# Kernel optimization log

Measured on AMD Instinct MI355X. Metric: run time of the kernel, lower is better.

Reference implementation:

```python
import jax, jax.numpy as jnp
import numpy as np

B, N, F, H, L = 8, 512, 32, 64, 2

def setup_inputs() -> dict:
    key = jax.random.key(0)
    ks = jax.random.split(key, 16)
    s = lambda fan_in: 1.0 / np.sqrt(fan_in)
    return {
        "x": jax.random.normal(ks[0], (B, N, F), dtype=jnp.float32),
        # node encoder: Linear(F, H), stored as [in, out]
        "W_enc": jax.random.uniform(ks[1], (F, H), minval=-s(F), maxval=s(F)),
        "b_enc": jax.random.uniform(ks[2], (H,), minval=-s(F), maxval=s(F)),
        # edge MLP: Linear(2H, H) then Linear(H, 1)
        "W_e1": jax.random.uniform(ks[3], (2 * H, H), minval=-s(2 * H), maxval=s(2 * H)),
        "b_e1": jax.random.uniform(ks[4], (H,), minval=-s(2 * H), maxval=s(2 * H)),
        "W_e2": jax.random.uniform(ks[5], (H,), minval=-s(H), maxval=s(H)),
        "b_e2": jax.random.uniform(ks[6], (), minval=-s(H), maxval=s(H)),
        # per-layer message Linear(H, H)
        "W_msg": jax.random.uniform(ks[7], (L, H, H), minval=-s(H), maxval=s(H)),
        "b_msg": jax.random.uniform(ks[8], (L, H), minval=-s(H), maxval=s(H)),
        # per-layer GRUCell(H, H): gates ordered [r, z, n], stored as [in, 3H]
        "W_ih": jax.random.uniform(ks[9], (L, H, 3 * H), minval=-s(H), maxval=s(H)),
        "b_ih": jax.random.uniform(ks[10], (L, 3 * H), minval=-s(H), maxval=s(H)),
        "W_hh": jax.random.uniform(ks[11], (L, H, 3 * H), minval=-s(H), maxval=s(H)),
        "b_hh": jax.random.uniform(ks[12], (L, 3 * H), minval=-s(H), maxval=s(H)),
        # output Linear(H, 1)
        "W_out": jax.random.uniform(ks[13], (H, 1), minval=-s(H), maxval=s(H)),
        "b_out": jax.random.uniform(ks[14], (1,), minval=-s(H), maxval=s(H)),
    }

def reference(x, W_enc, b_enc, W_e1, b_e1, W_e2, b_e2, W_msg, b_msg,
              W_ih, b_ih, W_hh, b_hh, W_out, b_out):
    # Node encoding (dropout is eval-mode identity)
    h = jax.nn.relu(x @ W_enc + b_enc)  # [B, N, H]

    # Edge MLP on pairwise concat [h_i, h_j]: split W_e1 so we never build the 2H concat
    Wa, Wb = W_e1[:H], W_e1[H:]
    zi = h @ Wa                           # contribution of h_i, [B, N, H]
    zj = h @ Wb                           # contribution of h_j, [B, N, H]
    e = jax.nn.relu(zi[:, :, None, :] + zj[:, None, :, :] + b_e1)  # [B, N, N, H]
    logits = jnp.einsum('bijh,h->bij', e, W_e2) + b_e2             # [B, N, N]

    eye = jnp.eye(logits.shape[-1], dtype=bool)
    logits = jnp.where(eye[None], -jnp.inf, logits)
    adj = jax.nn.softmax(logits, axis=-1)
    adj = jnp.nan_to_num(adj, nan=0.0, posinf=0.0, neginf=0.0)

    for l in range(L):
        m = jnp.einsum('bij,bjh->bih', adj, h)             # message aggregation
        m = jax.nn.relu(m @ W_msg[l] + b_msg[l])
        # GRUCell update (gates [r, z, n])
        gi = m @ W_ih[l] + b_ih[l]
        gh = h @ W_hh[l] + b_hh[l]
        ir, iz, inn = jnp.split(gi, 3, axis=-1)
        hr, hz, hn = jnp.split(gh, 3, axis=-1)
        r = jax.nn.sigmoid(ir + hr)
        z = jax.nn.sigmoid(iz + hz)
        n = jnp.tanh(inn + r * hn)
        h = (1.0 - z) * n + z * h

    graph_emb = jnp.mean(h, axis=1)       # [B, H]
    return graph_emb @ W_out + b_out      # [B, 1]
```

## Files before the change

kernel.cpp:

```cpp
#include <hip/hip_runtime.h>
#include <math.h>

#define BB 8
#define NN 512
#define FF 32
#define HH 64
#define NEG_BIG (-1.0e30f)

__device__ __forceinline__ float lane_bcast(float v, int l) {
    return __int_as_float(__builtin_amdgcn_readlane(__float_as_int(v), l));
}

__global__ __launch_bounds__(256) void encode_kernel(
    const float* __restrict__ x, const float* __restrict__ W_enc,
    const float* __restrict__ b_enc, const float* __restrict__ W_e1,
    const float* __restrict__ b_e1,
    float* __restrict__ h, float* __restrict__ zi, float* __restrict__ zj)
{
    const int t = threadIdx.x;
    const int hh = t & 63;
    const int qu = __builtin_amdgcn_readfirstlane(t >> 6);
    const int gR = blockIdx.x * 4 + qu;

    const float xv = x[gR * FF + (hh & 31)];
    float acc = b_enc[hh];
#pragma unroll 8
    for (int k = 0; k < FF; ++k)
        acc = fmaf(lane_bcast(xv, k), W_enc[k * HH + hh], acc);
    const float hval = fmaxf(acc, 0.f);
    h[gR * HH + hh] = hval;

    float z1 = b_e1[hh], z2 = 0.f;
#pragma unroll 8
    for (int k = 0; k < HH; ++k) {
        const float hk = lane_bcast(hval, k);
        z1 = fmaf(hk, W_e1[k * HH + hh], z1);
        z2 = fmaf(hk, W_e1[(HH + k) * HH + hh], z2);
    }
    zi[gR * HH + hh] = z1;
    zj[gR * HH + hh] = z2;
}

__global__ __launch_bounds__(256) void adj_kernel(
    const float* __restrict__ zi, const float* __restrict__ zj,
    const float* __restrict__ W_e2, const float* __restrict__ b_e2,
    float* __restrict__ adj)
{
    const int b = blockIdx.x >> 7;
    const int i0 = (blockIdx.x & 127) << 2;
    const int t = threadIdx.x;
    const int qu = __builtin_amdgcn_readfirstlane(t >> 6);
    const int tj = t & 63;
    const int j0 = (qu << 7) + tj;
    const int j1 = j0 + 64;

    __shared__ float zjs[NN][17];
    __shared__ float red[4][8];

    float zr[4];
#pragma unroll
    for (int r = 0; r < 4; ++r) zr[r] = zi[(b * NN + i0 + r) * HH + tj];
    const float wv = W_e2[tj];

    const float be2 = b_e2[0];
    float acc0[4], acc1[4];
#pragma unroll
    for (int r = 0; r < 4; ++r) { acc0[r] = be2; acc1[r] = be2; }

    for (int kp = 0; kp < 4; ++kp) {
        __syncthreads();
        {
            const int idx4 = t;
#pragma unroll
            for (int u = 0; u < 8; ++u) {
                const int i4 = idx4 + u * 256;
                const int row = i4 >> 2, c4 = i4 & 3;
                *(float4*)&zjs[row][c4 * 4] =
                    ((const float4*)(zj + (size_t)(b * NN + row) * HH))[kp * 4 + c4];
            }
        }
        __syncthreads();
#pragma unroll
        for (int c = 0; c < 16; ++c) {
            const int k = (kp << 4) + c;
            const float w = lane_bcast(wv, k);
            const float zj0 = zjs[j0][c];
            const float zj1 = zjs[j1][c];
#pragma unroll
            for (int r = 0; r < 4; ++r) {
                const float zv = lane_bcast(zr[r], k);
                acc0[r] = fmaf(fmaxf(zv + zj0, 0.f), w, acc0[r]);
                acc1[r] = fmaf(fmaxf(zv + zj1, 0.f), w, acc1[r]);
            }
        }
    }

#pragma unroll
    for (int r = 0; r < 4; ++r) {
        const int irow = i0 + r;
        if (j0 == irow) acc0[r] = NEG_BIG;
        if (j1 == irow) acc1[r] = NEG_BIG;
    }

    float wmax[4];
#pragma unroll
    for (int r = 0; r < 4; ++r) {
        float m = fmaxf(acc0[r], acc1[r]);
#pragma unroll
        for (int off = 32; off >= 1; off >>= 1) m = fmaxf(m, __shfl_xor(m, off));
        wmax[r] = m;
    }
    if (tj == 0) {
#pragma unroll
        for (int r = 0; r < 4; ++r) red[qu][r] = wmax[r];
    }
    __syncthreads();
    float M[4];
#pragma unroll
    for (int r = 0; r < 4; ++r)
        M[r] = fmaxf(fmaxf(red[0][r], red[1][r]), fmaxf(red[2][r], red[3][r]));
    __syncthreads();

    float e0[4], e1[4];
#pragma unroll
    for (int r = 0; r < 4; ++r) {
        e0[r] = __expf(acc0[r] - M[r]);
        e1[r] = __expf(acc1[r] - M[r]);
        float s = e0[r] + e1[r];
#pragma unroll
        for (int off = 32; off >= 1; off >>= 1) s += __shfl_xor(s, off);
        if (tj == 0) red[qu][r] = s;
    }
    __syncthreads();
#pragma unroll
    for (int r = 0; r < 4; ++r) {
        const float inv = 1.0f / (red[0][r] + red[1][r] + red[2][r] + red[3][r]);
        float* arow = adj + ((size_t)(b * NN + i0 + r)) * NN;
        arow[j0] = e0[r] * inv;
        arow[j1] = e1[r] * inv;
    }
}

__global__ __launch_bounds__(512, 4) void layer_kernel(
    const float* __restrict__ adjw, const float* __restrict__ h_in,
    const float* __restrict__ Wmsg, const float* __restrict__ bmsg,
    const float* __restrict__ Wih, const float* __restrict__ bih,
    const float* __restrict__ Whh, const float* __restrict__ bhh,
    float* __restrict__ h_out, float* __restrict__ partial)
{
    const int b  = blockIdx.x >> 6;
    const int i0 = (blockIdx.x & 63) << 3;
    const int t  = threadIdx.x;
    const int hh = t & 63;
    const int w  = __builtin_amdgcn_readfirstlane(t >> 6);
    const int gR0 = b * NN + i0;

    __shared__ float adjs[8][512];
    __shared__ union {
        float red[8][8][66];
        float gbuf[2][2][8][3][66];
    } U;
    __shared__ float mml[8][66];
    __shared__ float hol[8][66];

    {
        const float4* asrc = (const float4*)(adjw + (size_t)gR0 * NN);
        float4* adst = (float4*)&adjs[0][0];
        adst[t] = asrc[t];
        adst[t + 512] = asrc[t + 512];
    }
    hol[t >> 6][hh] = h_in[(size_t)(gR0 + (t >> 6)) * HH + hh];
    __syncthreads();

    {
        const float* hj = h_in + (size_t)b * NN * HH + (size_t)(w * 64) * HH + hh;
        float mac[8] = {0.f, 0.f, 0.f, 0.f, 0.f, 0.f, 0.f, 0.f};
#pragma unroll 2
        for (int j = 0; j < 64; j += 4) {
            const float h0 = hj[(j + 0) * HH];
            const float h1 = hj[(j + 1) * HH];
            const float h2 = hj[(j + 2) * HH];
            const float h3 = hj[(j + 3) * HH];
#pragma unroll
            for (int r = 0; r < 8; ++r) {
                const float4 av = *(const float4*)&adjs[r][w * 64 + j];
                mac[r] = fmaf(av.w, h3,
                         fmaf(av.z, h2,
                         fmaf(av.y, h1,
                         fmaf(av.x, h0, mac[r]))));
            }
        }
#pragma unroll
        for (int r = 0; r < 8; ++r) U.red[w][r][hh] = mac[r];
    }
    __syncthreads();

    {
        float m = 0.f;
#pragma unroll
        for (int p = 0; p < 8; ++p) m += U.red[p][w][hh];
        float acc = bmsg[hh];
#pragma unroll 4
        for (int k = 0; k < HH; ++k)
            acc = fmaf(lane_bcast(m, k), Wmsg[k * HH + hh], acc);
        mml[w][hh] = fmaxf(acc, 0.f);
    }
    __syncthreads();

    const int half = w >> 2, kh = (w >> 1) & 1, rq = w & 1;
    {
        const float* Wg = half ? Whh : Wih;
        const float* bg = half ? bhh : bih;
        float src[4];
#pragma unroll
        for (int r = 0; r < 4; ++r)
            src[r] = half ? hol[rq * 4 + r][hh] : mml[rq * 4 + r][hh];
        float a0[4], a1[4], a2[4];
#pragma unroll
        for (int r = 0; r < 4; ++r) {
            a0[r] = kh ? 0.f : bg[hh];
            a1[r] = kh ? 0.f : bg[64 + hh];
            a2[r] = kh ? 0.f : bg[128 + hh];
        }
        const int k0 = kh * 32;
#pragma unroll 2
        for (int kk = 0; kk < 32; ++kk) {
            const float* wk = Wg + (k0 + kk) * 192;
            const float w0 = wk[hh], w1 = wk[64 + hh], w2 = wk[128 + hh];
#pragma unroll
            for (int r = 0; r < 4; ++r) {
                const float v = lane_bcast(src[r], k0 + kk);
                a0[r] = fmaf(v, w0, a0[r]);
                a1[r] = fmaf(v, w1, a1[r]);
                a2[r] = fmaf(v, w2, a2[r]);
            }
        }
#pragma unroll
        for (int r = 0; r < 4; ++r) {
            U.gbuf[half][kh][rq * 4 + r][0][hh] = a0[r];
            U.gbuf[half][kh][rq * 4 + r][1][hh] = a1[r];
            U.gbuf[half][kh][rq * 4 + r][2][hh] = a2[r];
        }
    }
    __syncthreads();

    {
        const float ir = U.gbuf[0][0][w][0][hh] + U.gbuf[0][1][w][0][hh];
        const float iz = U.gbuf[0][0][w][1][hh] + U.gbuf[0][1][w][1][hh];
        const float in = U.gbuf[0][0][w][2][hh] + U.gbuf[0][1][w][2][hh];
        const float hr = U.gbuf[1][0][w][0][hh] + U.gbuf[1][1][w][0][hh];
        const float hz = U.gbuf[1][0][w][1][hh] + U.gbuf[1][1][w][1][hh];
        const float hn = U.gbuf[1][0][w][2][hh] + U.gbuf[1][1][w][2][hh];
        const float rr = 1.f / (1.f + __expf(-(ir + hr)));
        const float zz = 1.f / (1.f + __expf(-(iz + hz)));
        const float nnv = tanhf(in + rr * hn);
        const float hnew = (1.f - zz) * nnv + zz * hol[w][hh];
        h_out[(size_t)(gR0 + w) * HH + hh] = hnew;

        if (partial != nullptr) {
            __syncthreads();
            mml[w][hh] = hnew;
            __syncthreads();
            if (w == 0) {
                float s = 0.f;
#pragma unroll
                for (int r = 0; r < 8; ++r) s += mml[r][hh];
                partial[blockIdx.x * 64 + hh] = s;
            }
        }
    }
}

__global__ __launch_bounds__(64) void readout_kernel(
    const float* __restrict__ partial, const float* __restrict__ W_out,
    const float* __restrict__ b_out, float* __restrict__ out)
{
    const int b = blockIdx.x;
    const int hh = threadIdx.x;
    float s = 0.f;
#pragma unroll 8
    for (int c = 0; c < 64; ++c)
        s += partial[(b * 64 + c) * 64 + hh];
    float v = s * (1.0f / NN) * W_out[hh];
#pragma unroll
    for (int off = 32; off >= 1; off >>= 1) v += __shfl_xor(v, off);
    if (hh == 0) out[b] = v + b_out[0];
}

extern "C" void kernel_launch(void* const* d_in, const int* in_sizes, int n_in,
                              void* d_out, int out_size, void* d_ws, size_t ws_size,
                              hipStream_t stream)
{
    const float* x     = (const float*)d_in[0];
    const float* W_enc = (const float*)d_in[1];
    const float* b_enc = (const float*)d_in[2];
    const float* W_e1  = (const float*)d_in[3];
    const float* b_e1  = (const float*)d_in[4];
    const float* W_e2  = (const float*)d_in[5];
    const float* b_e2  = (const float*)d_in[6];
    const float* W_msg = (const float*)d_in[7];
    const float* b_msg = (const float*)d_in[8];
    const float* W_ih  = (const float*)d_in[9];
    const float* b_ih  = (const float*)d_in[10];
    const float* W_hh  = (const float*)d_in[11];
    const float* b_hh  = (const float*)d_in[12];
    const float* W_out = (const float*)d_in[13];
    const float* b_out = (const float*)d_in[14];
    float* out = (float*)d_out;

    float* ws  = (float*)d_ws;
    float* h0  = ws;
    float* h1  = h0 + BB * NN * HH;
    float* zi  = h1 + BB * NN * HH;
    float* zj  = zi + BB * NN * HH;
    float* prt = zj + BB * NN * HH;
    float* adjw = prt + 512 * 64;

    encode_kernel<<<BB * NN / 4, 256, 0, stream>>>(x, W_enc, b_enc, W_e1, b_e1, h0, zi, zj);
    adj_kernel<<<BB * (NN / 4), 256, 0, stream>>>(zi, zj, W_e2, b_e2, adjw);

    layer_kernel<<<BB * (NN / 8), 512, 0, stream>>>(
        adjw, h0, W_msg, b_msg, W_ih, b_ih, W_hh, b_hh, h1, nullptr);
    layer_kernel<<<BB * (NN / 8), 512, 0, stream>>>(
        adjw, h1, W_msg + HH * HH, b_msg + HH,
        W_ih + HH * 3 * HH, b_ih + 3 * HH, W_hh + HH * 3 * HH, b_hh + 3 * HH,
        h0, prt);

    readout_kernel<<<BB, 64, 0, stream>>>(prt, W_out, b_out, out);
}
```

Baseline: 79.02 us.

## Fuse adjacency softmax into first GNN layer kernel and keep adj in registers

Merges the adjacency-logit/softmax kernel into the first message-passing layer, so each 256-thread block computes 8 rows of adj, writes them out for layer 2, and uses the register-held values directly for aggregation via lane broadcasts. This removes one launch and the global re-read of adj in layer 1. The layer kernel is also restructured from 512 to 256 threads with 2 rows per wave and shared memory reused between phases. The cost is higher register pressure, and the adj compute now runs on half as many blocks with 8 rows each, which may reduce parallelism.

```diff
diff --git a/kernel.cpp b/kernel.cpp
--- a/kernel.cpp
+++ b/kernel.cpp
@@ -41,108 +41,11 @@
     zj[gR * HH + hh] = z2;
 }
 
-__global__ __launch_bounds__(256) void adj_kernel(
+template <int MODE>
+__global__ __launch_bounds__(256, 2) void adjlayer_kernel(
     const float* __restrict__ zi, const float* __restrict__ zj,
-    const float* __restrict__ W_e2, const float* __restrict__ b_e2,
-    float* __restrict__ adj)
-{
-    const int b = blockIdx.x >> 7;
-    const int i0 = (blockIdx.x & 127) << 2;
-    const int t = threadIdx.x;
-    const int qu = __builtin_amdgcn_readfirstlane(t >> 6);
-    const int tj = t & 63;
-    const int j0 = (qu << 7) + tj;
-    const int j1 = j0 + 64;
-
-    __shared__ float zjs[NN][17];
-    __shared__ float red[4][8];
-
-    float zr[4];
-#pragma unroll
-    for (int r = 0; r < 4; ++r) zr[r] = zi[(b * NN + i0 + r) * HH + tj];
-    const float wv = W_e2[tj];
-
-    const float be2 = b_e2[0];
-    float acc0[4], acc1[4];
-#pragma unroll
-    for (int r = 0; r < 4; ++r) { acc0[r] = be2; acc1[r] = be2; }
-
-    for (int kp = 0; kp < 4; ++kp) {
-        __syncthreads();
-        {
-            const int idx4 = t;
-#pragma unroll
-            for (int u = 0; u < 8; ++u) {
-                const int i4 = idx4 + u * 256;
-                const int row = i4 >> 2, c4 = i4 & 3;
-                *(float4*)&zjs[row][c4 * 4] =
-                    ((const float4*)(zj + (size_t)(b * NN + row) * HH))[kp * 4 + c4];
-            }
-        }
-        __syncthreads();
-#pragma unroll
-        for (int c = 0; c < 16; ++c) {
-            const int k = (kp << 4) + c;
-            const float w = lane_bcast(wv, k);
-            const float zj0 = zjs[j0][c];
-            const float zj1 = zjs[j1][c];
-#pragma unroll
-            for (int r = 0; r < 4; ++r) {
-                const float zv = lane_bcast(zr[r], k);
-                acc0[r] = fmaf(fmaxf(zv + zj0, 0.f), w, acc0[r]);
-                acc1[r] = fmaf(fmaxf(zv + zj1, 0.f), w, acc1[r]);
-            }
-        }
-    }
-
-#pragma unroll
-    for (int r = 0; r < 4; ++r) {
-        const int irow = i0 + r;
-        if (j0 == irow) acc0[r] = NEG_BIG;
-        if (j1 == irow) acc1[r] = NEG_BIG;
-    }
-
-    float wmax[4];
-#pragma unroll
-    for (int r = 0; r < 4; ++r) {
-        float m = fmaxf(acc0[r], acc1[r]);
-#pragma unroll
-        for (int off = 32; off >= 1; off >>= 1) m = fmaxf(m, __shfl_xor(m, off));
-        wmax[r] = m;
-    }
-    if (tj == 0) {
-#pragma unroll
-        for (int r = 0; r < 4; ++r) red[qu][r] = wmax[r];
-    }
-    __syncthreads();
-    float M[4];
-#pragma unroll
-    for (int r = 0; r < 4; ++r)
-        M[r] = fmaxf(fmaxf(red[0][r], red[1][r]), fmaxf(red[2][r], red[3][r]));
-    __syncthreads();
-
-    float e0[4], e1[4];
-#pragma unroll
-    for (int r = 0; r < 4; ++r) {
-        e0[r] = __expf(acc0[r] - M[r]);
-        e1[r] = __expf(acc1[r] - M[r]);
-        float s = e0[r] + e1[r];
-#pragma unroll
-        for (int off = 32; off >= 1; off >>= 1) s += __shfl_xor(s, off);
-        if (tj == 0) red[qu][r] = s;
-    }
-    __syncthreads();
-#pragma unroll
-    for (int r = 0; r < 4; ++r) {
-        const float inv = 1.0f / (red[0][r] + red[1][r] + red[2][r] + red[3][r]);
-        float* arow = adj + ((size_t)(b * NN + i0 + r)) * NN;
-        arow[j0] = e0[r] * inv;
-        arow[j1] = e1[r] * inv;
-    }
-}
-
-__global__ __launch_bounds__(512, 4) void layer_kernel(
-    const float* __restrict__ adjw, const float* __restrict__ h_in,
+    const float* __restrict__ We2, const float* __restrict__ be2,
+    float* __restrict__ adjw, const float* __restrict__ h_in,
     const float* __restrict__ Wmsg, const float* __restrict__ bmsg,
     const float* __restrict__ Wih, const float* __restrict__ bih,
     const float* __restrict__ Whh, const float* __restrict__ bhh,
@@ -151,124 +54,215 @@
     const int b  = blockIdx.x >> 6;
     const int i0 = (blockIdx.x & 63) << 3;
     const int t  = threadIdx.x;
-    const int hh = t & 63;
+    const int tj = t & 63;
     const int w  = __builtin_amdgcn_readfirstlane(t >> 6);
     const int gR0 = b * NN + i0;
 
-    __shared__ float adjs[8][512];
-    __shared__ union {
-        float red[8][8][66];
-        float gbuf[2][2][8][3][66];
-    } U;
+    __shared__ float smem[NN * 17];
     __shared__ float mml[8][66];
     __shared__ float hol[8][66];
+    __shared__ float redm[4][8];
+    __shared__ float reds[4][8];
+
+    float (*zjs)[17] = (float (*)[17])smem;
+#define RED(p, r, c)       smem[(((p) * 8) + (r)) * 66 + (c)]
+#define GP(h2, k2, r, g, c) smem[((((((h2) * 2 + (k2)) * 8) + (r)) * 3 + (g)) * 66) + (c)]
+
+    const int r0 = 2 * w, r1 = 2 * w + 1;
+    hol[r0][tj] = h_in[(size_t)(gR0 + r0) * HH + tj];
+    hol[r1][tj] = h_in[(size_t)(gR0 + r1) * HH + tj];
+
+    float va[8][2];
+    if (MODE == 0) {
+        float zir[8];
+#pragma unroll
+        for (int r = 0; r < 8; ++r) zir[r] = zi[(size_t)(gR0 + r) * HH + tj];
+        const float wv = We2[tj];
+        const float bias2 = be2[0];
+        float acc[8][2];
+#pragma unroll
+        for (int r = 0; r < 8; ++r) { acc[r][0] = bias2; acc[r][1] = bias2; }
+
+        for (int kp = 0; kp < 4; ++kp) {
+            __syncthreads();
+#pragma unroll
+            for (int u = 0; u < 8; ++u) {
+                const int i4 = t + u * 256;
+                const int row = i4 >> 2, c4 = i4 & 3;
+                *(float4*)&zjs[row][c4 * 4] =
+                    ((const float4*)(zj + (size_t)(b * NN + row) * HH))[kp * 4 + c4];
+            }
+            __syncthreads();
+            const int j0 = 128 * w + tj, j1 = j0 + 64;
+#pragma unroll
+            for (int kk = 0; kk < 16; ++kk) {
+                const int k = (kp << 4) + kk;
+                const float wk = lane_bcast(wv, k);
+                const float zj0 = zjs[j0][kk];
+                const float zj1 = zjs[j1][kk];
+#pragma unroll
+                for (int r = 0; r < 8; ++r) {
+                    const float zv = lane_bcast(zir[r], k);
+                    acc[r][0] = fmaf(fmaxf(zv + zj0, 0.f), wk, acc[r][0]);
+                    acc[r][1] = fmaf(fmaxf(zv + zj1, 0.f), wk, acc[r][1]);
+                }
+            }
+        }
+#pragma unroll
+        for (int r = 0; r < 8; ++r)
+#pragma unroll
+            for (int c = 0; c < 2; ++c)
+                if (128 * w + 64 * c + tj == i0 + r) acc[r][c] = NEG_BIG;
+
+#pragma unroll
+        for (int r = 0; r < 8; ++r) {
+            float m = fmaxf(acc[r][0], acc[r][1]);
+#pragma unroll
+            for (int off = 32; off >= 1; off >>= 1) m = fmaxf(m, __shfl_xor(m, off));
+            if (tj == 0) redm[w][r] = m;
+        }
+        __syncthreads();
+        float M[8];
+#pragma unroll
+        for (int r = 0; r < 8; ++r)
+            M[r] = fmaxf(fmaxf(redm[0][r], redm[1][r]),
+                         fmaxf(redm[2][r], redm[3][r]));
+#pragma unroll
+        for (int r = 0; r < 8; ++r) {
+            const float e0 = __expf(acc[r][0] - M[r]);
+            const float e1 = __expf(acc[r][1] - M[r]);
+            va[r][0] = e0; va[r][1] = e1;
+            float s = e0 + e1;
+#pragma unroll
+            for (int off = 32; off >= 1; off >>= 1) s += __shfl_xor(s, off);
+            if (tj == 0) reds[w][r] = s;
+        }
+        __syncthreads();
+#pragma unroll
+        for (int r = 0; r < 8; ++r) {
+            const float inv = 1.0f /
+                (reds[0][r] + reds[1][r] + reds[2][r] + reds[3][r]);
+            va[r][0] *= inv; va[r][1] *= inv;
+            adjw[(size_t)(gR0 + r) * NN + 128 * w + tj]      = va[r][0];
+            adjw[(size_t)(gR0 + r) * NN + 128 * w + 64 + tj] = va[r][1];
+        }
+    } else {
+#pragma unroll
+        for (int r = 0; r < 8; ++r) {
+            va[r][0] = adjw[(size_t)(gR0 + r) * NN + 128 * w + tj];
+            va[r][1] = adjw[(size_t)(gR0 + r) * NN + 128 * w + 64 + tj];
+        }
+    }
 
     {
-        const float4* asrc = (const float4*)(adjw + (size_t)gR0 * NN);
-        float4* adst = (float4*)&adjs[0][0];
-        adst[t] = asrc[t];
-        adst[t + 512] = asrc[t + 512];
-    }
-    hol[t >> 6][hh] = h_in[(size_t)(gR0 + (t >> 6)) * HH + hh];
+        const float* hq = h_in + ((size_t)b * NN + 128 * w) * HH + tj;
+        float mac[8] = {0.f, 0.f, 0.f, 0.f, 0.f, 0.f, 0.f, 0.f};
+#pragma unroll
+        for (int c = 0; c < 2; ++c) {
+#pragma unroll 4
+            for (int jj = 0; jj < 64; jj += 4) {
+                const float h0 = hq[(64 * c + jj + 0) * HH];
+                const float h1 = hq[(64 * c + jj + 1) * HH];
+                const float h2 = hq[(64 * c + jj + 2) * HH];
+                const float h3 = hq[(64 * c + jj + 3) * HH];
+#pragma unroll
+                for (int r = 0; r < 8; ++r) {
+                    float a = fmaf(lane_bcast(va[r][c], jj + 0), h0, mac[r]);
+                    a = fmaf(lane_bcast(va[r][c], jj + 1), h1, a);
+                    a = fmaf(lane_bcast(va[r][c], jj + 2), h2, a);
+                    mac[r] = fmaf(lane_bcast(va[r][c], jj + 3), h3, a);
+                }
+            }
+        }
+        if (MODE == 0) __syncthreads();
+#pragma unroll
+        for (int r = 0; r < 8; ++r) RED(w, r, tj) = mac[r];
+    }
     __syncthreads();
 
+    float mm0, mm1;
     {
-        const float* hj = h_in + (size_t)b * NN * HH + (size_t)(w * 64) * HH + hh;
-        float mac[8] = {0.f, 0.f, 0.f, 0.f, 0.f, 0.f, 0.f, 0.f};
-#pragma unroll 2
-        for (int j = 0; j < 64; j += 4) {
-            const float h0 = hj[(j + 0) * HH];
-            const float h1 = hj[(j + 1) * HH];
-            const float h2 = hj[(j + 2) * HH];
-            const float h3 = hj[(j + 3) * HH];
-#pragma unroll
-            for (int r = 0; r < 8; ++r) {
-                const float4 av = *(const float4*)&adjs[r][w * 64 + j];
-                mac[r] = fmaf(av.w, h3,
-                         fmaf(av.z, h2,
-                         fmaf(av.y, h1,
-                         fmaf(av.x, h0, mac[r]))));
-            }
-        }
-#pragma unroll
-        for (int r = 0; r < 8; ++r) U.red[w][r][hh] = mac[r];
+        const float m0 = RED(0, r0, tj) + RED(1, r0, tj) + RED(2, r0, tj) + RED(3, r0, tj);
+        const float m1 = RED(0, r1, tj) + RED(1, r1, tj) + RED(2, r1, tj) + RED(3, r1, tj);
+        mm0 = bmsg[tj]; mm1 = mm0;
+#pragma unroll 8
+        for (int k = 0; k < HH; ++k) {
+            const float wm = Wmsg[k * HH + tj];
+            mm0 = fmaf(lane_bcast(m0, k), wm, mm0);
+            mm1 = fmaf(lane_bcast(m1, k), wm, mm1);
+        }
+        mm0 = fmaxf(mm0, 0.f); mm1 = fmaxf(mm1, 0.f);
+        mml[r0][tj] = mm0; mml[r1][tj] = mm1;
     }
     __syncthreads();
 
     {
-        float m = 0.f;
-#pragma unroll
-        for (int p = 0; p < 8; ++p) m += U.red[p][w][hh];
-        float acc = bmsg[hh];
-#pragma unroll 4
-        for (int k = 0; k < HH; ++k)
-            acc = fmaf(lane_bcast(m, k), Wmsg[k * HH + hh], acc);
-        mml[w][hh] = fmaxf(acc, 0.f);
-    }
-    __syncthreads();
-
-    const int half = w >> 2, kh = (w >> 1) & 1, rq = w & 1;
-    {
+        const int half = w >> 1, kh = w & 1;
         const float* Wg = half ? Whh : Wih;
         const float* bg = half ? bhh : bih;
-        float src[4];
-#pragma unroll
-        for (int r = 0; r < 4; ++r)
-            src[r] = half ? hol[rq * 4 + r][hh] : mml[rq * 4 + r][hh];
-        float a0[4], a1[4], a2[4];
-#pragma unroll
-        for (int r = 0; r < 4; ++r) {
-            a0[r] = kh ? 0.f : bg[hh];
-            a1[r] = kh ? 0.f : bg[64 + hh];
-            a2[r] = kh ? 0.f : bg[128 + hh];
+        float sreg[8];
+#pragma unroll
+        for (int r = 0; r < 8; ++r) sreg[r] = half ? hol[r][tj] : mml[r][tj];
+        float g0[8], g1[8], g2[8];
+#pragma unroll
+        for (int r = 0; r < 8; ++r) {
+            g0[r] = kh ? 0.f : bg[tj];
+            g1[r] = kh ? 0.f : bg[64 + tj];
+            g2[r] = kh ? 0.f : bg[128 + tj];
         }
         const int k0 = kh * 32;
-#pragma unroll 2
+#pragma unroll 4
         for (int kk = 0; kk < 32; ++kk) {
-            const float* wk = Wg + (k0 + kk) * 192;
-            const float w0 = wk[hh], w1 = wk[64 + hh], w2 = wk[128 + hh];
-#pragma unroll
-            for (int r = 0; r < 4; ++r) {
-                const float v = lane_bcast(src[r], k0 + kk);
-                a0[r] = fmaf(v, w0, a0[r]);
-                a1[r] = fmaf(v, w1, a1[r]);
-                a2[r] = fmaf(v, w2, a2[r]);
+            const float* wk = Wg + (size_t)(k0 + kk) * 192;
+            const float w0 = wk[tj], w1 = wk[64 + tj], w2 = wk[128 + tj];
+#pragma unroll
+            for (int r = 0; r < 8; ++r) {
+                const float s = lane_bcast(sreg[r], k0 + kk);
+                g0[r] = fmaf(s, w0, g0[r]);
+                g1[r] = fmaf(s, w1, g1[r]);
+                g2[r] = fmaf(s, w2, g2[r]);
             }
         }
 #pragma unroll
-        for (int r = 0; r < 4; ++r) {
-            U.gbuf[half][kh][rq * 4 + r][0][hh] = a0[r];
-            U.gbuf[half][kh][rq * 4 + r][1][hh] = a1[r];
-            U.gbuf[half][kh][rq * 4 + r][2][hh] = a2[r];
+        for (int r = 0; r < 8; ++r) {
+            GP(half, kh, r, 0, tj) = g0[r];
+            GP(half, kh, r, 1, tj) = g1[r];
+            GP(half, kh, r, 2, tj) = g2[r];
         }
     }
     __syncthreads();
 
-    {
-        const float ir = U.gbuf[0][0][w][0][hh] + U.gbuf[0][1][w][0][hh];
-        const float iz = U.gbuf[0][0][w][1][hh] + U.gbuf[0][1][w][1][hh];
-        const float in = U.gbuf[0][0][w][2][hh] + U.gbuf[0][1][w][2][hh];
-        const float hr = U.gbuf[1][0][w][0][hh] + U.gbuf[1][1][w][0][hh];
-        const float hz = U.gbuf[1][0][w][1][hh] + U.gbuf[1][1][w][1][hh];
-        const float hn = U.gbuf[1][0][w][2][hh] + U.gbuf[1][1][w][2][hh];
-        const float rr = 1.f / (1.f + __expf(-(ir + hr)));
-        const float zz = 1.f / (1.f + __expf(-(iz + hz)));
-        const float nnv = tanhf(in + rr * hn);
-        const float hnew = (1.f - zz) * nnv + zz * hol[w][hh];
-        h_out[(size_t)(gR0 + w) * HH + hh] = hnew;
-
-        if (partial != nullptr) {
-            __syncthreads();
-            mml[w][hh] = hnew;
-            __syncthreads();
-            if (w == 0) {
-                float s = 0.f;
-#pragma unroll
-                for (int r = 0; r < 8; ++r) s += mml[r][hh];
-                partial[blockIdx.x * 64 + hh] = s;
-            }
-        }
-    }
+    float hs0 = 0.f, hs1 = 0.f;
+#pragma unroll
+    for (int p = 0; p < 2; ++p) {
+        const int rr = p ? r1 : r0;
+        const float ir  = GP(0, 0, rr, 0, tj) + GP(0, 1, rr, 0, tj);
+        const float iz  = GP(0, 0, rr, 1, tj) + GP(0, 1, rr, 1, tj);
+        const float inn = GP(0, 0, rr, 2, tj) + GP(0, 1, rr, 2, tj);
+        const float hr  = GP(1, 0, rr, 0, tj) + GP(1, 1, rr, 0, tj);
+        const float hz  = GP(1, 0, rr, 1, tj) + GP(1, 1, rr, 1, tj);
+        const float hn  = GP(1, 0, rr, 2, tj) + GP(1, 1, rr, 2, tj);
+        const float rg = 1.f / (1.f + __expf(-(ir + hr)));
+        const float zg = 1.f / (1.f + __expf(-(iz + hz)));
+        const float ng = tanhf(inn + rg * hn);
+        const float hnew = (1.f - zg) * ng + zg * hol[rr][tj];
+        h_out[(size_t)(gR0 + rr) * HH + tj] = hnew;
+        if (p) hs1 = hnew; else hs0 = hnew;
+    }
+
+    if (MODE == 1) {
+        __syncthreads();
+        mml[r0][tj] = hs0; mml[r1][tj] = hs1;
+        __syncthreads();
+        if (w == 0) {
+            float s = 0.f;
+#pragma unroll
+            for (int r = 0; r < 8; ++r) s += mml[r][tj];
+            partial[blockIdx.x * 64 + tj] = s;
+        }
+    }
+#undef RED
+#undef GP
 }
 
 __global__ __launch_bounds__(64) void readout_kernel(
@@ -317,12 +311,13 @@
     float* adjw = prt + 512 * 64;
 
     encode_kernel<<<BB * NN / 4, 256, 0, stream>>>(x, W_enc, b_enc, W_e1, b_e1, h0, zi, zj);
-    adj_kernel<<<BB * (NN / 4), 256, 0, stream>>>(zi, zj, W_e2, b_e2, adjw);
-
-    layer_kernel<<<BB * (NN / 8), 512, 0, stream>>>(
-        adjw, h0, W_msg, b_msg, W_ih, b_ih, W_hh, b_hh, h1, nullptr);
-    layer_kernel<<<BB * (NN / 8), 512, 0, stream>>>(
-        adjw, h1, W_msg + HH * HH, b_msg + HH,
+
+    adjlayer_kernel<0><<<BB * (NN / 8), 256, 0, stream>>>(
+        zi, zj, W_e2, b_e2, adjw, h0,
+        W_msg, b_msg, W_ih, b_ih, W_hh, b_hh, h1, nullptr);
+    adjlayer_kernel<1><<<BB * (NN / 8), 256, 0, stream>>>(
+        zi, zj, W_e2, b_e2, adjw, h1,
+        W_msg + HH * HH, b_msg + HH,
         W_ih + HH * 3 * HH, b_ih + 3 * HH, W_hh + HH * 3 * HH, b_hh + 3 * HH,
         h0, prt);
 
```

Result: slower. 82.92 us (+4.9%).
